# Performance work log

Hardware: AMD Instinct MI355X
Metric: run time of the kernel (lower is better)

The kernel has to match this reference:

```python
import jax, jax.numpy as jnp
import numpy as np

NC = 6            # CPAB tessellation cells (tess_size=6, zero_boundary=True)
DIM = NC - 1      # theta dimension = 5
SIG_LEN = 2048
CHANNELS = 3
BATCH = 256
FC_IN = 64 * 168  # flattened net_part1 output for signal_len=2048
NUM_SCALING = 0   # N in transform_data_ss
EPS_BN = 1e-5


def _cpab_basis():
    """QR null-space basis of the CPAB continuity + zero-boundary constraints.
    Params ordered [a_1,b_1,...,a_NC,b_NC]; v(x)=a_c x + b_c on cell c."""
    nc = NC
    L = np.zeros((nc + 1, 2 * nc))
    for k in range(1, nc):  # continuity at internal knots x_k = k/nc
        xk = k / nc
        L[k - 1, 2 * (k - 1)] = xk
        L[k - 1, 2 * (k - 1) + 1] = 1.0
        L[k - 1, 2 * k] = -xk
        L[k - 1, 2 * k + 1] = -1.0
    L[nc - 1, 1] = 1.0        # v(0) = 0  -> b_1 = 0
    L[nc, 2 * (nc - 1)] = 1.0  # v(1) = 0 -> a_nc + b_nc = 0
    L[nc, 2 * nc - 1] = 1.0
    Q, _ = np.linalg.qr(L.T, mode='complete')
    return np.ascontiguousarray(Q[:, nc + 1:]).astype(np.float32)  # (12, 5)


def _conv1d(x, w, b):
    y = jax.lax.conv_general_dilated(x, w, (1,), 'VALID',
                                     dimension_numbers=('NCH', 'OIH', 'NCH'))
    return y + b[None, :, None]


def _maxpool1d(x, k, s):
    return jax.lax.reduce_window(x, -jnp.inf, jax.lax.max, (1, 1, k), (1, 1, s), 'VALID')


def _bn(x, g, b, m, v):  # eval-mode BatchNorm1d
    return (x - m[None, :, None]) * (g / jnp.sqrt(v + EPS_BN))[None, :, None] + b[None, :, None]


def _integrate(x, A):
    """Exact CPAB 1D flow integration over t=1 with cell-crossing handling.
    x: (B, n) points in [0,1]; A: (B, NC, 2) per-cell (a, b). Monotone
    trajectories cross at most NC-1 boundaries -> fixed NC+1 iterations."""
    a_all, b_all = A[:, :, 0], A[:, :, 1]
    t = jnp.ones_like(x)
    for _ in range(NC + 1):
        c = jnp.clip(jnp.floor(x * NC).astype(jnp.int32), 0, NC - 1)
        a = jnp.take_along_axis(a_all, c, axis=1)
        b = jnp.take_along_axis(b_all, c, axis=1)
        v = a * x + b
        xb = jnp.where(v >= 0, (c + 1).astype(x.dtype) / NC, c.astype(x.dtype) / NC)
        big_a = jnp.abs(a) > 1e-8
        a_s = jnp.where(big_a, a, 1.0)
        z = x + b / a_s        # shifted coord: x(t) = z*exp(a t) - b/a
        zb = xb + b / a_s
        ratio = zb / jnp.where(jnp.abs(z) > 1e-12, z, 1e-12)
        t_exp = jnp.log(jnp.maximum(ratio, 1e-12)) / a_s
        v_s = jnp.where(jnp.abs(v) > 1e-12, v, 1.0)
        t_lin = (xb - x) / v_s
        thit = jnp.where(big_a, t_exp, t_lin)
        valid = (jnp.abs(v) > 1e-12) & (thit > 0) & (jnp.where(big_a, ratio, 1.0) > 0)
        thit = jnp.where(valid, thit, jnp.inf)
        tau = jnp.minimum(t, thit)
        x_new = jnp.where(big_a, z * jnp.exp(a * tau) - (z - x), x + b * tau)
        hit = thit <= t
        nudge = jnp.where(v >= 0, 1e-6, -1e-6)  # push into next cell
        x = jnp.clip(jnp.where(hit, xb + nudge, x_new), 0.0, 1.0)
        t = jnp.maximum(t - tau, 0.0)
    return x


def _interp1d(data, pos):
    """data: (B, L, C); pos: (B, n) in [0,1] -> (B, n, C) linear interpolation."""
    Lw = data.shape[1]
    p = jnp.clip(pos, 0.0, 1.0) * (Lw - 1)
    x0 = jnp.clip(jnp.floor(p).astype(jnp.int32), 0, Lw - 2)
    w = (p - x0.astype(p.dtype))[:, :, None]
    d0 = jnp.take_along_axis(data, x0[:, :, None], axis=1)
    d1 = jnp.take_along_axis(data, (x0 + 1)[:, :, None], axis=1)
    return d0 * (1.0 - w) + d1 * w


def _transform_data_ss(data, theta, basis, outsize, N):
    """CPAB scaling-and-squaring warp of data (B, L, C) by theta (B, DIM)."""
    Bsz = theta.shape[0]
    A = (theta @ basis.T).reshape(Bsz, NC, 2) / (2.0 ** N)
    grid = jnp.linspace(0.0, 1.0, outsize, dtype=data.dtype)
    grid_t = _integrate(jnp.broadcast_to(grid, (Bsz, outsize)), A)
    for _ in range(N):  # squaring: compose the warp with itself
        grid_t = _interp1d(grid_t[:, :, None], grid_t)[:, :, 0]
    return _interp1d(data, grid_t)


def reference(x, conv1_w, conv1_b, bn1_g, bn1_b, bn1_m, bn1_v,
              conv2_w, conv2_b, bn2_g, bn2_b, bn2_m, bn2_v,
              conv3_w, conv3_b, bn3_g, bn3_b, bn3_m, bn3_v,
              fc1_w, fc1_b, fc2_w, fc2_b, fc3_w, fc3_b, fc4_w, fc4_b, basis):
    # localization net (n_recurrence = 1, back_version = True)
    h = jax.nn.relu(_maxpool1d(_bn(_conv1d(x, conv1_w, conv1_b), bn1_g, bn1_b, bn1_m, bn1_v), 3, 2))
    h = jax.nn.relu(_maxpool1d(_bn(_conv1d(h, conv2_w, conv2_b), bn2_g, bn2_b, bn2_m, bn2_v), 3, 3))
    h = jax.nn.relu(_maxpool1d(_bn(_conv1d(h, conv3_w, conv3_b), bn3_g, bn3_b, bn3_m, bn3_v), 3, 2))
    xs = h.reshape(h.shape[0], -1)  # (B, 64*168)
    xs = jax.nn.relu(xs @ fc1_w.T + fc1_b)
    xs = jax.nn.relu(xs @ fc2_w.T + fc2_b)
    xs = jax.nn.relu(xs @ fc3_w.T + fc3_b)
    theta = jnp.tanh(xs @ fc4_w.T + fc4_b)  # (B, 5)
    data = jnp.transpose(x, (0, 2, 1))       # (B, L, C)
    warped = _transform_data_ss(data, theta, basis, SIG_LEN, NUM_SCALING)
    return jnp.transpose(warped, (0, 2, 1))  # (B, C, L)


def setup_inputs() -> dict:
    key = jax.random.key(0)
    ks = jax.random.split(key, 16)
    def nrm(k, shape, scale):
        return (jax.random.normal(k, shape) * scale).astype(jnp.float32)
    inp = {}
    inp['x'] = jax.random.normal(ks[0], (BATCH, CHANNELS, SIG_LEN), dtype=jnp.float32)
    inp['conv1_w'] = nrm(ks[1], (128, CHANNELS, 3), (CHANNELS * 3) ** -0.5)
    inp['conv1_b'] = nrm(ks[2], (128,), 0.01)
    inp['bn1_g'] = jnp.ones((128,), jnp.float32)
    inp['bn1_b'] = jnp.zeros((128,), jnp.float32)
    inp['bn1_m'] = nrm(ks[3], (128,), 0.1)
    inp['bn1_v'] = jnp.ones((128,), jnp.float32)
    inp['conv2_w'] = nrm(ks[4], (64, 128, 5), (128 * 5) ** -0.5)
    inp['conv2_b'] = nrm(ks[5], (64,), 0.01)
    inp['bn2_g'] = jnp.ones((64,), jnp.float32)
    inp['bn2_b'] = jnp.zeros((64,), jnp.float32)
    inp['bn2_m'] = nrm(ks[6], (64,), 0.1)
    inp['bn2_v'] = jnp.ones((64,), jnp.float32)
    inp['conv3_w'] = nrm(ks[7], (64, 64, 3), (64 * 3) ** -0.5)
    inp['conv3_b'] = nrm(ks[8], (64,), 0.01)
    inp['bn3_g'] = jnp.ones((64,), jnp.float32)
    inp['bn3_b'] = jnp.zeros((64,), jnp.float32)
    inp['bn3_m'] = nrm(ks[9], (64,), 0.1)
    inp['bn3_v'] = jnp.ones((64,), jnp.float32)
    inp['fc1_w'] = nrm(ks[10], (48, FC_IN), FC_IN ** -0.5)
    inp['fc1_b'] = jnp.zeros((48,), jnp.float32)
    inp['fc2_w'] = nrm(ks[11], (32, 48), 48 ** -0.5)
    inp['fc2_b'] = jnp.zeros((32,), jnp.float32)
    inp['fc3_w'] = nrm(ks[12], (16, 32), 32 ** -0.5)
    inp['fc3_b'] = jnp.zeros((16,), jnp.float32)
    # near-identity warp head (original zero-inits weight, identity bias)
    inp['fc4_w'] = nrm(ks[13], (DIM, 16), 0.01)
    inp['fc4_b'] = nrm(ks[14], (DIM,), 0.01)
    inp['basis'] = jnp.asarray(_cpab_basis())
    return inp
```

## Files before the change

### kernel.cpp

```cpp
#include <hip/hip_runtime.h>
#include <math.h>

#define BATCH   256
#define SIGLEN  2048
#define L1OUT   1022
#define L2OUT   339
#define L3OUT   168
#define FCIN    10752

#define TP2   32
#define NROW  100
#define PLANE (NROW*128)

#define TU3   28

typedef float f32x4   __attribute__((ext_vector_type(4)));
typedef float f32x16  __attribute__((ext_vector_type(16)));
typedef short s16x8   __attribute__((ext_vector_type(8)));

__device__ __forceinline__ unsigned short f2bf(float f) {
    unsigned int u = __float_as_uint(f);
    return (unsigned short)((u + 0x7fffu + ((u >> 16) & 1u)) >> 16);
}
__device__ __forceinline__ float bf2f(unsigned short h) {
    return __uint_as_float(((unsigned int)h) << 16);
}

__launch_bounds__(256)
__global__ void prep_kernel(
    const float* __restrict__ conv1_b,
    const float* __restrict__ g1, const float* __restrict__ b1,
    const float* __restrict__ m1, const float* __restrict__ v1,
    const float* __restrict__ conv2_w, const float* __restrict__ conv2_b,
    const float* __restrict__ g2, const float* __restrict__ b2,
    const float* __restrict__ m2, const float* __restrict__ v2,
    const float* __restrict__ conv3_w, const float* __restrict__ conv3_b,
    const float* __restrict__ g3, const float* __restrict__ b3,
    const float* __restrict__ m3, const float* __restrict__ v3,
    const float* __restrict__ fc1_w,
    unsigned short* __restrict__ w2hi, unsigned short* __restrict__ w2lo,
    unsigned short* __restrict__ w3hi, unsigned short* __restrict__ w3lo,
    float* __restrict__ wp1,
    float* __restrict__ so1, float* __restrict__ so2, float* __restrict__ so3)
{
    __shared__ float tl[64 * 169];

    int t   = threadIdx.x;
    int tid = blockIdx.x * 256 + t;
    int stride = gridDim.x * 256;

    if (blockIdx.x < 48) {
        int o = blockIdx.x;
        for (int i = t; i < FCIN; i += 256) {
            int co = i / L3OUT, u = i - co * L3OUT;
            tl[co * 169 + u] = fc1_w[o * FCIN + i];
        }
        __syncthreads();
        for (int i = t; i < FCIN; i += 256) {
            int u = i >> 6, co = i & 63;
            wp1[o * FCIN + i] = tl[co * 169 + u];
        }
    }

    for (int i = tid; i < 64*128*5; i += stride) {
        int co = i / 640; int rr = i - co*640; int ci = rr / 5; int k = rr - ci*5;
        float w = conv2_w[i];
        unsigned short hi = f2bf(w);
        unsigned short lo = f2bf(w - bf2f(hi));
        int dst = ((k*8 + (ci >> 4))*64 + co)*16 + (ci & 15);
        w2hi[dst] = hi;
        w2lo[dst] = lo;
    }
    for (int i = tid; i < 64*64*3; i += stride) {
        int co = i / 192; int r = i - co*192; int ci = r / 3; int k = r - ci*3;
        float w = conv3_w[i];
        unsigned short hi = f2bf(w);
        unsigned short lo = f2bf(w - bf2f(hi));
        int dst = ((k*2 + (ci >> 5))*64 + co)*32 + (ci & 31);
        w3hi[dst] = hi;
        w3lo[dst] = lo;
    }
    if (tid < 128) {
        float s = g1[tid] / sqrtf(v1[tid] + 1e-5f);
        so1[tid]       = s;
        so1[128 + tid] = (conv1_b[tid] - m1[tid]) * s + b1[tid];
    }
    if (tid < 64) {
        float s2 = g2[tid] / sqrtf(v2[tid] + 1e-5f);
        so2[tid]      = s2;
        so2[64 + tid] = (conv2_b[tid] - m2[tid]) * s2 + b2[tid];
        float s3 = g3[tid] / sqrtf(v3[tid] + 1e-5f);
        so3[tid]      = s3;
        so3[64 + tid] = (conv3_b[tid] - m3[tid]) * s3 + b3[tid];
    }
}

__launch_bounds__(512, 6)
__global__ void conv12_kernel(
    const float* __restrict__ x, const float* __restrict__ w1,
    const unsigned short* __restrict__ w2hi, const unsigned short* __restrict__ w2lo,
    const float* __restrict__ so1, const float* __restrict__ so2,
    unsigned int* __restrict__ h2p)
{
    __shared__ unsigned short h1[2*PLANE];
    unsigned short* h1hi = h1;
    unsigned short* h1lo = h1 + PLANE;

    int t  = threadIdx.x;
    int b  = blockIdx.x;
    int by = blockIdx.y;
    int u0 = by * TP2;
    int wv = __builtin_amdgcn_readfirstlane(t >> 6);
    int l  = t & 63;

    {
        float wr[2][9], s1r[2], o1r[2];
        #pragma unroll
        for (int h = 0; h < 2; ++h) {
            int ch = 2*l + h;
            #pragma unroll
            for (int j = 0; j < 9; ++j) wr[h][j] = w1[ch*9 + j];
            s1r[h] = so1[ch]; o1r[h] = so1[128 + ch];
        }

        int rbase = 13 * wv;
        int W0 = 192*by + 2*rbase;
        const float* xp0 = x + b*3*SIGLEN;

        float xv[3][6];
        if (W0 + 5 <= SIGLEN - 1) {
            #pragma unroll
            for (int ci = 0; ci < 3; ++ci) {
                const float* xp = xp0 + ci*SIGLEN + W0;
                float2 v01 = *(const float2*)(xp);
                float2 v23 = *(const float2*)(xp + 2);
                float2 v45 = *(const float2*)(xp + 4);
                xv[ci][0] = v01.x; xv[ci][1] = v01.y;
                xv[ci][2] = v23.x; xv[ci][3] = v23.y;
                xv[ci][4] = v45.x; xv[ci][5] = v45.y;
            }
        } else {
            #pragma unroll
            for (int ci = 0; ci < 3; ++ci)
                #pragma unroll
                for (int j = 0; j < 6; ++j) {
                    int xi = W0 + j; xi = xi < SIGLEN ? xi : SIGLEN - 1;
                    xv[ci][j] = xp0[ci*SIGLEN + xi];
                }
        }

        float cr0 = 0.f, cr1 = 0.f;
        #pragma unroll
        for (int s = 0; s < 13; ++s) {
            int r = rbase + s;
            if (r < NROW) {
                float vo[2];
                #pragma unroll
                for (int h = 0; h < 2; ++h) {
                    float r0, r1 = 0.f, r2 = 0.f;
                    if (s == 0) {
                        r0 = 0.f;
                        #pragma unroll
                        for (int ci = 0; ci < 3; ++ci)
                            r0 = fmaf(xv[ci][0], wr[h][ci*3],
                                 fmaf(xv[ci][1], wr[h][ci*3+1],
                                 fmaf(xv[ci][2], wr[h][ci*3+2], r0)));
                    } else {
                        r0 = h ? cr1 : cr0;
                    }
                    #pragma unroll
                    for (int ci = 0; ci < 3; ++ci) {
                        float wA = wr[h][ci*3], wB = wr[h][ci*3+1], wC = wr[h][ci*3+2];
                        r1 = fmaf(xv[ci][1], wA, fmaf(xv[ci][2], wB, fmaf(xv[ci][3], wC, r1)));
                        r2 = fmaf(xv[ci][2], wA, fmaf(xv[ci][3], wB, fmaf(xv[ci][4], wC, r2)));
                    }
                    if (h) cr1 = r2; else cr0 = r2;
                    float mx = fmaxf(r0, fmaxf(r1, r2));
                    vo[h] = fmaxf(fmaf(s1r[h], mx, o1r[h]), 0.f);
                }
                unsigned ua = __float_as_uint(vo[0]);
                unsigned ub = __float_as_uint(vo[1]);
                unsigned hb = ub & 0xffff0000u;
                unsigned hipack = (ua >> 16) | hb;
                float ra = vo[0] - __uint_as_float(ua & 0xffff0000u);
                float rb = vo[1] - __uint_as_float(hb);
                unsigned lopack = (__float_as_uint(ra) >> 16) | (__float_as_uint(rb) & 0xffff0000u);
                int wi = r*64 + (l ^ ((r & 7) << 2));
                ((unsigned*)h1hi)[wi] = hipack;
                ((unsigned*)h1lo)[wi] = lopack;
            }
            if (s < 12) {
                #pragma unroll
                for (int ci = 0; ci < 3; ++ci) {
                    xv[ci][0] = xv[ci][2]; xv[ci][1] = xv[ci][3];
                    xv[ci][2] = xv[ci][4]; xv[ci][3] = xv[ci][5];
                }
                int Wn = W0 + 2*s + 6;
                if (Wn + 1 <= SIGLEN - 1) {
                    #pragma unroll
                    for (int ci = 0; ci < 3; ++ci) {
                        float2 v = *(const float2*)(xp0 + ci*SIGLEN + Wn);
                        xv[ci][4] = v.x; xv[ci][5] = v.y;
                    }
                } else {
                    #pragma unroll
                    for (int ci = 0; ci < 3; ++ci) {
                        int x4 = Wn     < SIGLEN ? Wn     : SIGLEN - 1;
                        int x5 = Wn + 1 < SIGLEN ? Wn + 1 : SIGLEN - 1;
                        xv[ci][4] = xp0[ci*SIGLEN + x4];
                        xv[ci][5] = xp0[ci*SIGLEN + x5];
                    }
                }
            }
        }
    }
    __syncthreads();

    int tid8 = (wv + ((b + by) & 7)) & 7;
    int active = tid8 < 6;
    int mt = tid8 >> 1;
    int nt = tid8 & 1;
    int lm  = l & 31;
    int hi8 = (l >> 5) * 8;

    f32x16 acc = (f32x16)(0.f);
    if (active) {
        const unsigned short* wbh = w2hi + (nt*32 + lm)*16 + hi8;
        const unsigned short* wbl = w2lo + (nt*32 + lm)*16 + hi8;
        #pragma unroll
        for (int k = 0; k < 5; ++k) {
            int row = mt*32 + lm + k;
            int sb  = row*128 + hi8;
            int swz = (row & 7) << 3;
            #pragma unroll
            for (int c16 = 0; c16 < 8; ++c16) {
                int st = k*8 + c16;
                s16x8 wh = *(const s16x8*)(wbh + st*1024);
                s16x8 wl = *(const s16x8*)(wbl + st*1024);
                int idx = (sb + c16*16) ^ swz;
                s16x8 ah = *(const s16x8*)&h1hi[idx];
                s16x8 al = *(const s16x8*)&h1lo[idx];
                acc = __builtin_amdgcn_mfma_f32_32x32x16_bf16(ah, wh, acc, 0, 0, 0);
                acc = __builtin_amdgcn_mfma_f32_32x32x16_bf16(al, wh, acc, 0, 0, 0);
                acc = __builtin_amdgcn_mfma_f32_32x32x16_bf16(ah, wl, acc, 0, 0, 0);
            }
        }
    }
    __syncthreads();

    float* c2 = (float*)h1;
    if (active) {
        #pragma unroll
        for (int rg = 0; rg < 16; ++rg) {
            int prow = mt*32 + (rg & 3) + 8*(rg >> 2) + 4*(l >> 5);
            c2[prow*65 + nt*32 + lm] = acc[rg];
        }
    }
    __syncthreads();

    #pragma unroll
    for (int it = 0; it < 4; ++it) {
        int idx = t + it*512;
        int ul = idx >> 6, co = idx & 63;
        int u = u0 + ul;
        if (u < L2OUT) {
            float v0 = c2[(3*ul  )*65 + co];
            float v1 = c2[(3*ul+1)*65 + co];
            float v2 = c2[(3*ul+2)*65 + co];
            float mm = fmaxf(v0, fmaxf(v1, v2));
            float v  = fmaxf(fmaf(so2[co], mm, so2[64 + co]), 0.f);
            unsigned uu = __float_as_uint(v);
            float rr = v - __uint_as_float(uu & 0xffff0000u);
            h2p[(b*L2OUT + u)*64 + co] = (uu >> 16) | (__float_as_uint(rr) & 0xffff0000u);
        }
    }
}

__launch_bounds__(256, 4)
__global__ void conv3fc1_kernel(
    const unsigned int* __restrict__ h2p,
    const unsigned short* __restrict__ w3hi, const unsigned short* __restrict__ w3lo,
    const float* __restrict__ so3, const float* __restrict__ wp1,
    float* __restrict__ part)
{
    __shared__ unsigned short h3s[2*66*72];
    __shared__ float c3buf[64*65];

    int t  = threadIdx.x;
    int b  = blockIdx.x;
    int ti = blockIdx.y;
    int u0 = ti * TU3;
    int wv = __builtin_amdgcn_readfirstlane(t >> 6);
    int l  = t & 63;
    int m  = l & 15;
    int qd = l >> 4;

    for (int i = t; i < 66*64; i += 256) {
        int r = i >> 6, ci = i & 63;
        int g = 2*u0 + r; g = g > (L2OUT-1) ? (L2OUT-1) : g;
        unsigned int v = h2p[(b*L2OUT + g)*64 + ci];
        h3s[r*72 + ci]         = (unsigned short)(v & 0xffffu);
        h3s[66*72 + r*72 + ci] = (unsigned short)(v >> 16);
    }
    __syncthreads();

    s16x8 wh[6], wl[6];
    #pragma unroll
    for (int s = 0; s < 6; ++s) {
        wh[s] = *(const s16x8*)(w3hi + s*2048 + (wv*16 + m)*32 + qd*8);
        wl[s] = *(const s16x8*)(w3lo + s*2048 + (wv*16 + m)*32 + qd*8);
    }

    f32x4 acc[4] = {(f32x4)(0.f), (f32x4)(0.f), (f32x4)(0.f), (f32x4)(0.f)};
    #pragma unroll
    for (int pt = 0; pt < 4; ++pt) {
        #pragma unroll
        for (int s = 0; s < 6; ++s) {
            int row = pt*16 + m + (s >> 1);
            int off = (s & 1)*32 + qd*8;
            s16x8 ah = *(const s16x8*)&h3s[row*72 + off];
            s16x8 al = *(const s16x8*)&h3s[66*72 + row*72 + off];
            acc[pt] = __builtin_amdgcn_mfma_f32_16x16x32_bf16(ah, wh[s], acc[pt], 0, 0, 0);
            acc[pt] = __builtin_amdgcn_mfma_f32_16x16x32_bf16(al, wh[s], acc[pt], 0, 0, 0);
            acc[pt] = __builtin_amdgcn_mfma_f32_16x16x32_bf16(ah, wl[s], acc[pt], 0, 0, 0);
        }
    }
    __syncthreads();

    #pragma unroll
    for (int pt = 0; pt < 4; ++pt)
        #pragma unroll
        for (int rg = 0; rg < 4; ++rg)
            c3buf[(pt*16 + qd*4 + rg)*65 + wv*16 + m] = acc[pt][rg];
    __syncthreads();

    float s3 = so3[l], o3 = so3[64 + l];
    float pooled[TU3];
    #pragma unroll
    for (int u = 0; u < TU3; ++u) {
        int p = 2*u;
        float v0 = c3buf[(p  )*65 + l];
        float v1 = c3buf[(p+1)*65 + l];
        float v2 = c3buf[(p+2)*65 + l];
        pooled[u] = fmaxf(fmaf(s3, fmaxf(v0, fmaxf(v1, v2)), o3), 0.f);
    }

    int o0 = wv * 12;
    float fa[12];
    #pragma unroll
    for (int j = 0; j < 12; ++j) fa[j] = 0.f;
    #pragma unroll 4
    for (int u = 0; u < TU3; ++u) {
        float pv = pooled[u];
        const float* wp = wp1 + (u0 + u)*64 + l;
        #pragma unroll
        for (int j = 0; j < 12; ++j)
            fa[j] = fmaf(pv, wp[(o0 + j)*FCIN], fa[j]);
    }
    #pragma unroll
    for (int j = 0; j < 12; ++j) {
        #pragma unroll
        for (int off = 32; off > 0; off >>= 1)
            fa[j] += __shfl_xor(fa[j], off, 64);
    }
    if (l == 0) {
        #pragma unroll
        for (int j = 0; j < 12; ++j)
            part[(b*6 + ti)*48 + o0 + j] = fa[j];
    }
}

__launch_bounds__(256)
__global__ void warp_kernel(
    const float* __restrict__ x, const float* __restrict__ part,
    const float* __restrict__ fc1_b,
    const float* __restrict__ fc2_w, const float* __restrict__ fc2_b,
    const float* __restrict__ fc3_w, const float* __restrict__ fc3_b,
    const float* __restrict__ fc4_w, const float* __restrict__ fc4_b,
    const float* __restrict__ basis,
    float* __restrict__ out)
{
    __shared__ float xs48[48], hl[32], gl[16], thl[5], Al[12];

    int b = blockIdx.x;
    int t = threadIdx.x;

    if (t < 48) {
        float sv = 0.f;
        #pragma unroll
        for (int ti = 0; ti < 6; ++ti) sv += part[(b*6 + ti)*48 + t];
        xs48[t] = fmaxf(sv + fc1_b[t], 0.f);
    }
    __syncthreads();
    if (t < 32) {
        float sv = fc2_b[t];
        #pragma unroll
        for (int k = 0; k < 48; ++k) sv = fmaf(fc2_w[t * 48 + k], xs48[k], sv);
        hl[t] = fmaxf(sv, 0.f);
    }
    __syncthreads();
    if (t < 16) {
        float sv = fc3_b[t];
        #pragma unroll
        for (int k = 0; k < 32; ++k) sv = fmaf(fc3_w[t * 32 + k], hl[k], sv);
        gl[t] = fmaxf(sv, 0.f);
    }
    __syncthreads();
    if (t < 5) {
        float sv = fc4_b[t];
        #pragma unroll
        for (int k = 0; k < 16; ++k) sv = fmaf(fc4_w[t * 16 + k], gl[k], sv);
        thl[t] = tanhf(sv);
    }
    __syncthreads();
    if (t < 12) {
        float sv = 0.f;
        #pragma unroll
        for (int d = 0; d < 5; ++d) sv = fmaf(basis[t * 5 + d], thl[d], sv);
        Al[t] = sv;
    }
    __syncthreads();

    float a_r[6], b_r[6];
    #pragma unroll
    for (int c = 0; c < 6; ++c) { a_r[c] = Al[2*c]; b_r[c] = Al[2*c+1]; }

    #pragma unroll
    for (int cc = 0; cc < 2; ++cc) {
        int i = (blockIdx.y * 2 + cc) * 256 + t;
        float xp = (float)i / 2047.f;
        float tt = 1.f;
        for (int it = 0; it < 7; ++it) {
            int c = (int)floorf(xp * 6.f);
            c = min(max(c, 0), 5);
            float a  = a_r[c], bb = b_r[c];
            float v  = a * xp + bb;
            float xb = (v >= 0.f) ? (float)(c + 1) / 6.f : (float)c / 6.f;
            bool  big_a = fabsf(a) > 1e-8f;
            float a_s = big_a ? a : 1.f;
            float z   = xp + bb / a_s;
            float zb  = xb + bb / a_s;
            float zden = (fabsf(z) > 1e-12f) ? z : 1e-12f;
            float ratio = zb / zden;
            float t_exp = logf(fmaxf(ratio, 1e-12f)) / a_s;
            float v_s   = (fabsf(v) > 1e-12f) ? v : 1.f;
            float t_lin = (xb - xp) / v_s;
            float thit  = big_a ? t_exp : t_lin;
            bool valid  = (fabsf(v) > 1e-12f) && (thit > 0.f) && ((big_a ? ratio : 1.f) > 0.f);
            if (!valid) thit = __builtin_inff();
            float tau   = fminf(tt, thit);
            float x_new = big_a ? (z * expf(a * tau) - (z - xp)) : (xp + bb * tau);
            bool hit    = (thit <= tt);
            float nudge = (v >= 0.f) ? 1e-6f : -1e-6f;
            xp = hit ? (xb + nudge) : x_new;
            xp = fminf(fmaxf(xp, 0.f), 1.f);
            tt = fmaxf(tt - tau, 0.f);
        }
        float p = fminf(fmaxf(xp, 0.f), 1.f) * 2047.f;
        int i0 = (int)floorf(p);
        i0 = min(max(i0, 0), 2046);
        float w = p - (float)i0;
        #pragma unroll
        for (int c = 0; c < 3; ++c) {
            const float* d = &x[(b * 3 + c) * SIGLEN];
            out[(b * 3 + c) * SIGLEN + i] = d[i0] * (1.f - w) + d[i0 + 1] * w;
        }
    }
}

extern "C" void kernel_launch(void* const* d_in, const int* in_sizes, int n_in,
                              void* d_out, int out_size, void* d_ws, size_t ws_size,
                              hipStream_t stream) {
    (void)in_sizes; (void)n_in; (void)out_size; (void)ws_size;
    const float* x       = (const float*)d_in[0];
    const float* conv1_w = (const float*)d_in[1];
    const float* conv1_b = (const float*)d_in[2];
    const float* bn1_g   = (const float*)d_in[3];
    const float* bn1_b   = (const float*)d_in[4];
    const float* bn1_m   = (const float*)d_in[5];
    const float* bn1_v   = (const float*)d_in[6];
    const float* conv2_w = (const float*)d_in[7];
    const float* conv2_b = (const float*)d_in[8];
    const float* bn2_g   = (const float*)d_in[9];
    const float* bn2_b   = (const float*)d_in[10];
    const float* bn2_m   = (const float*)d_in[11];
    const float* bn2_v   = (const float*)d_in[12];
    const float* conv3_w = (const float*)d_in[13];
    const float* conv3_b = (const float*)d_in[14];
    const float* bn3_g   = (const float*)d_in[15];
    const float* bn3_b   = (const float*)d_in[16];
    const float* bn3_m   = (const float*)d_in[17];
    const float* bn3_v   = (const float*)d_in[18];
    const float* fc1_w   = (const float*)d_in[19];
    const float* fc1_b   = (const float*)d_in[20];
    const float* fc2_w   = (const float*)d_in[21];
    const float* fc2_b   = (const float*)d_in[22];
    const float* fc3_w   = (const float*)d_in[23];
    const float* fc3_b   = (const float*)d_in[24];
    const float* fc4_w   = (const float*)d_in[25];
    const float* fc4_b   = (const float*)d_in[26];
    const float* basis   = (const float*)d_in[27];

    unsigned short* w2hi = (unsigned short*)d_ws;
    unsigned short* w2lo = w2hi + 40960;
    unsigned short* w3hi = w2lo + 40960;
    unsigned short* w3lo = w3hi + 12288;
    float* ws   = (float*)d_ws;
    float* so1  = ws + 53248;
    float* so2  = so1 + 256;
    float* so3  = so2 + 128;
    float* wp1  = so3 + 128;
    unsigned int* h2p = (unsigned int*)(wp1 + 516096);
    float* part = (float*)(h2p + 5554176);

    prep_kernel<<<128, 256, 0, stream>>>(
        conv1_b, bn1_g, bn1_b, bn1_m, bn1_v,
        conv2_w, conv2_b, bn2_g, bn2_b, bn2_m, bn2_v,
        conv3_w, conv3_b, bn3_g, bn3_b, bn3_m, bn3_v,
        fc1_w, w2hi, w2lo, w3hi, w3lo, wp1, so1, so2, so3);

    dim3 g2(BATCH, (L2OUT + TP2 - 1) / TP2);
    conv12_kernel<<<g2, 512, 0, stream>>>(x, conv1_w, w2hi, w2lo, so1, so2, h2p);

    dim3 g3(BATCH, 6);
    conv3fc1_kernel<<<g3, 256, 0, stream>>>(h2p, w3hi, w3lo, so3, wp1, part);

    dim3 g5(BATCH, 4);
    warp_kernel<<<g5, 256, 0, stream>>>(x, part, fc1_b, fc2_w, fc2_b,
                                        fc3_w, fc3_b, fc4_w, fc4_b, basis,
                                        (float*)d_out);
}
```

Baseline: 250.0 us.

## Split conv2 MFMA work along K across waves and reduce partials in LDS

Each active wave now covers all three M tiles for one third of the 40 K steps, where before it handled one M tile over all K steps. Each B fragment (weight) load is reused across three MFMA tiles and is prefetched one step ahead. The partial accumulators are then combined through an LDS reduction with an extra barrier. This trades fewer global weight loads for triple the accumulator registers, extra LDS traffic and a sync, and the loop is no longer unrolled.

```diff
diff --git a/kernel.cpp b/kernel.cpp
--- a/kernel.cpp
+++ b/kernel.cpp
@@ -218,31 +218,61 @@
 
     int tid8 = (wv + ((b + by) & 7)) & 7;
     int active = tid8 < 6;
-    int mt = tid8 >> 1;
     int nt = tid8 & 1;
+    int j  = tid8 >> 1;
     int lm  = l & 31;
     int hi8 = (l >> 5) * 8;
 
-    f32x16 acc = (f32x16)(0.f);
+    f32x16 acc[3] = {(f32x16)(0.f), (f32x16)(0.f), (f32x16)(0.f)};
     if (active) {
+        int st  = (j == 0) ? 0 : (j == 1 ? 14 : 27);
+        int cnt = (j == 0) ? 14 : 13;
         const unsigned short* wbh = w2hi + (nt*32 + lm)*16 + hi8;
         const unsigned short* wbl = w2lo + (nt*32 + lm)*16 + hi8;
-        #pragma unroll
-        for (int k = 0; k < 5; ++k) {
-            int row = mt*32 + lm + k;
-            int sb  = row*128 + hi8;
-            int swz = (row & 7) << 3;
+        s16x8 wh = *(const s16x8*)(wbh + st*1024);
+        s16x8 wl = *(const s16x8*)(wbl + st*1024);
+        for (int i = 0; i < cnt; ++i) {
+            int stn = st + 1; stn = stn > 39 ? 39 : stn;
+            s16x8 whn = *(const s16x8*)(wbh + stn*1024);
+            s16x8 wln = *(const s16x8*)(wbl + stn*1024);
+            int k = st >> 3, c16 = st & 7;
+            int rb = lm + k;
             #pragma unroll
-            for (int c16 = 0; c16 < 8; ++c16) {
-                int st = k*8 + c16;
-                s16x8 wh = *(const s16x8*)(wbh + st*1024);
-                s16x8 wl = *(const s16x8*)(wbl + st*1024);
-                int idx = (sb + c16*16) ^ swz;
+            for (int mt = 0; mt < 3; ++mt) {
+                int row = mt*32 + rb;
+                int idx = (row*128 + c16*16 + hi8) ^ ((row & 7) << 3);
                 s16x8 ah = *(const s16x8*)&h1hi[idx];
                 s16x8 al = *(const s16x8*)&h1lo[idx];
-                acc = __builtin_amdgcn_mfma_f32_32x32x16_bf16(ah, wh, acc, 0, 0, 0);
-                acc = __builtin_amdgcn_mfma_f32_32x32x16_bf16(al, wh, acc, 0, 0, 0);
-                acc = __builtin_amdgcn_mfma_f32_32x32x16_bf16(ah, wl, acc, 0, 0, 0);
+                acc[mt] = __builtin_amdgcn_mfma_f32_32x32x16_bf16(ah, wh, acc[mt], 0, 0, 0);
+                acc[mt] = __builtin_amdgcn_mfma_f32_32x32x16_bf16(al, wh, acc[mt], 0, 0, 0);
+                acc[mt] = __builtin_amdgcn_mfma_f32_32x32x16_bf16(ah, wl, acc[mt], 0, 0, 0);
+            }
+            wh = whn; wl = wln; st = stn;
+        }
+    }
+    __syncthreads();
+
+    float* P = (float*)h1;
+    if (active) {
+        #pragma unroll
+        for (int mt = 0; mt < 3; ++mt) {
+            if (mt != j) {
+                int slot = ((mt + 1) % 3 == j) ? 0 : 1;
+                float* dst = P + ((nt*3 + mt)*2 + slot)*1024 + l;
+                #pragma unroll
+                for (int rg = 0; rg < 16; ++rg) dst[rg*64] = acc[mt][rg];
+            }
+        }
+    }
+    __syncthreads();
+    if (active) {
+        #pragma unroll
+        for (int mt = 0; mt < 3; ++mt) {
+            if (mt == j) {
+                const float* s0 = P + ((nt*3 + mt)*2 + 0)*1024 + l;
+                #pragma unroll
+                for (int rg = 0; rg < 16; ++rg)
+                    acc[mt][rg] += s0[rg*64] + s0[1024 + rg*64];
             }
         }
     }
@@ -251,9 +281,14 @@
     float* c2 = (float*)h1;
     if (active) {
         #pragma unroll
-        for (int rg = 0; rg < 16; ++rg) {
-            int prow = mt*32 + (rg & 3) + 8*(rg >> 2) + 4*(l >> 5);
-            c2[prow*65 + nt*32 + lm] = acc[rg];
+        for (int mt = 0; mt < 3; ++mt) {
+            if (mt == j) {
+                #pragma unroll
+                for (int rg = 0; rg < 16; ++rg) {
+                    int prow = mt*32 + (rg & 3) + 8*(rg >> 2) + 4*(l >> 5);
+                    c2[prow*65 + nt*32 + lm] = acc[mt][rg];
+                }
+            }
         }
     }
     __syncthreads();
```

Result: no change. 252.6 us (+1.1%).

## Warp-specialize conv12 into persistent per-batch block with double-buffered conv1 producer

Applied to the files above, without the earlier changes.

The conv1+conv2 kernel becomes one 1024-thread block per batch element that walks all 11 position tiles, in place of a 2D grid of 512-thread blocks. Four waves act as producers and compute the next tile's conv1 rows into a double-buffered LDS plane while twelve MFMA waves compute conv2 on the current tile. The conv2 K dimension is split across wave pairs and the halves are summed in LDS. This aims to overlap the scalar conv1 work with matrix-core work and to use all waves, where six of eight were active before. In exchange it adds more barriers, raises LDS use, and gives the grid only 256 blocks.

```diff
diff --git a/kernel.cpp b/kernel.cpp
--- a/kernel.cpp
+++ b/kernel.cpp
@@ -11,6 +11,7 @@
 #define TP2   32
 #define NROW  100
 #define PLANE (NROW*128)
+#define NTILE 11
 
 #define TU3   28
 
@@ -95,26 +96,140 @@
     }
 }
 
-__launch_bounds__(512, 6)
+__device__ __forceinline__ void c1_init_window(const float* xp0, int W0, float xv[3][6])
+{
+    if (W0 + 5 <= SIGLEN - 1) {
+        #pragma unroll
+        for (int ci = 0; ci < 3; ++ci) {
+            const float* xp = xp0 + ci*SIGLEN + W0;
+            float2 v01 = *(const float2*)(xp);
+            float2 v23 = *(const float2*)(xp + 2);
+            float2 v45 = *(const float2*)(xp + 4);
+            xv[ci][0] = v01.x; xv[ci][1] = v01.y;
+            xv[ci][2] = v23.x; xv[ci][3] = v23.y;
+            xv[ci][4] = v45.x; xv[ci][5] = v45.y;
+        }
+    } else {
+        #pragma unroll
+        for (int ci = 0; ci < 3; ++ci)
+            #pragma unroll
+            for (int j = 0; j < 6; ++j) {
+                int xi = W0 + j; xi = xi < SIGLEN ? xi : SIGLEN - 1;
+                xv[ci][j] = xp0[ci*SIGLEN + xi];
+            }
+    }
+}
+
+__device__ __forceinline__ void c1_row(
+    const float* xp0, int W0, int r, bool fresh, bool refill, int s,
+    const float wr[2][9], const float s1r[2], const float o1r[2],
+    float xv[3][6], float& cr0, float& cr1,
+    unsigned* dhi, unsigned* dlo, int l)
+{
+    float vo[2];
+    #pragma unroll
+    for (int h = 0; h < 2; ++h) {
+        float r0;
+        if (fresh) {
+            r0 = 0.f;
+            #pragma unroll
+            for (int ci = 0; ci < 3; ++ci)
+                r0 = fmaf(xv[ci][0], wr[h][ci*3],
+                     fmaf(xv[ci][1], wr[h][ci*3+1],
+                     fmaf(xv[ci][2], wr[h][ci*3+2], r0)));
+        } else {
+            r0 = h ? cr1 : cr0;
+        }
+        float r1 = 0.f, r2 = 0.f;
+        #pragma unroll
+        for (int ci = 0; ci < 3; ++ci) {
+            float wA = wr[h][ci*3], wB = wr[h][ci*3+1], wC = wr[h][ci*3+2];
+            r1 = fmaf(xv[ci][1], wA, fmaf(xv[ci][2], wB, fmaf(xv[ci][3], wC, r1)));
+            r2 = fmaf(xv[ci][2], wA, fmaf(xv[ci][3], wB, fmaf(xv[ci][4], wC, r2)));
+        }
+        if (h) cr1 = r2; else cr0 = r2;
+        float mx = fmaxf(r0, fmaxf(r1, r2));
+        vo[h] = fmaxf(fmaf(s1r[h], mx, o1r[h]), 0.f);
+    }
+    unsigned ua = __float_as_uint(vo[0]);
+    unsigned ub = __float_as_uint(vo[1]);
+    unsigned hb = ub & 0xffff0000u;
+    unsigned hipack = (ua >> 16) | hb;
+    float ra = vo[0] - __uint_as_float(ua & 0xffff0000u);
+    float rb = vo[1] - __uint_as_float(hb);
+    unsigned lopack = (__float_as_uint(ra) >> 16) | (__float_as_uint(rb) & 0xffff0000u);
+    int wi = r*64 + (l ^ ((r & 7) << 2));
+    dhi[wi] = hipack;
+    dlo[wi] = lopack;
+    if (refill) {
+        #pragma unroll
+        for (int ci = 0; ci < 3; ++ci) {
+            xv[ci][0] = xv[ci][2]; xv[ci][1] = xv[ci][3];
+            xv[ci][2] = xv[ci][4]; xv[ci][3] = xv[ci][5];
+        }
+        int Wn = W0 + 2*s + 6;
+        if (Wn + 1 <= SIGLEN - 1) {
+            #pragma unroll
+            for (int ci = 0; ci < 3; ++ci) {
+                float2 v = *(const float2*)(xp0 + ci*SIGLEN + Wn);
+                xv[ci][4] = v.x; xv[ci][5] = v.y;
+            }
+        } else {
+            #pragma unroll
+            for (int ci = 0; ci < 3; ++ci) {
+                int x4 = Wn     < SIGLEN ? Wn     : SIGLEN - 1;
+                int x5 = Wn + 1 < SIGLEN ? Wn + 1 : SIGLEN - 1;
+                xv[ci][4] = xp0[ci*SIGLEN + x4];
+                xv[ci][5] = xp0[ci*SIGLEN + x5];
+            }
+        }
+    }
+}
+
+__device__ __forceinline__ void c1_seg(
+    int s0, int s1, int tile, int g, int l, const float* xp0,
+    const float wr[2][9], const float s1r[2], const float o1r[2],
+    float xv[3][6], float& cr0, float& cr1,
+    unsigned short* bhi, unsigned short* blo)
+{
+    int rbase = g * 25;
+    int W0 = 192*tile + 2*rbase;
+    unsigned* dhi = (unsigned*)bhi;
+    unsigned* dlo = (unsigned*)blo;
+    if (s0 == 0) {
+        c1_init_window(xp0, W0, xv);
+        c1_row(xp0, W0, rbase, true, true, 0, wr, s1r, o1r, xv, cr0, cr1, dhi, dlo, l);
+        for (int s = 1; s < s1; ++s)
+            c1_row(xp0, W0, rbase + s, false, true, s, wr, s1r, o1r, xv, cr0, cr1, dhi, dlo, l);
+    } else {
+        for (int s = s0; s < s1; ++s)
+            c1_row(xp0, W0, rbase + s, false, s < 24, s, wr, s1r, o1r, xv, cr0, cr1, dhi, dlo, l);
+    }
+}
+
+__launch_bounds__(1024, 4)
 __global__ void conv12_kernel(
     const float* __restrict__ x, const float* __restrict__ w1,
     const unsigned short* __restrict__ w2hi, const unsigned short* __restrict__ w2lo,
     const float* __restrict__ so1, const float* __restrict__ so2,
     unsigned int* __restrict__ h2p)
 {
-    __shared__ unsigned short h1[2*PLANE];
-    unsigned short* h1hi = h1;
-    unsigned short* h1lo = h1 + PLANE;
+    __shared__ unsigned short h1[2][2*PLANE];
+    __shared__ float c2s[96*65];
 
     int t  = threadIdx.x;
     int b  = blockIdx.x;
-    int by = blockIdx.y;
-    int u0 = by * TP2;
     int wv = __builtin_amdgcn_readfirstlane(t >> 6);
     int l  = t & 63;
 
-    {
-        float wr[2][9], s1r[2], o1r[2];
+    float so2s = so2[t & 63], so2o = so2[64 + (t & 63)];
+
+    float wr[2][9], s1r[2], o1r[2];
+    float xv[3][6];
+    float cr0 = 0.f, cr1 = 0.f;
+    int g = wv - 12;
+    const float* xp0 = x + b*3*SIGLEN;
+    if (wv >= 12) {
         #pragma unroll
         for (int h = 0; h < 2; ++h) {
             int ch = 2*l + h;
@@ -122,157 +237,86 @@
             for (int j = 0; j < 9; ++j) wr[h][j] = w1[ch*9 + j];
             s1r[h] = so1[ch]; o1r[h] = so1[128 + ch];
         }
-
-        int rbase = 13 * wv;
-        int W0 = 192*by + 2*rbase;
-        const float* xp0 = x + b*3*SIGLEN;
-
-        float xv[3][6];
-        if (W0 + 5 <= SIGLEN - 1) {
-            #pragma unroll
-            for (int ci = 0; ci < 3; ++ci) {
-                const float* xp = xp0 + ci*SIGLEN + W0;
-                float2 v01 = *(const float2*)(xp);
-                float2 v23 = *(const float2*)(xp + 2);
-                float2 v45 = *(const float2*)(xp + 4);
-                xv[ci][0] = v01.x; xv[ci][1] = v01.y;
-                xv[ci][2] = v23.x; xv[ci][3] = v23.y;
-                xv[ci][4] = v45.x; xv[ci][5] = v45.y;
-            }
-        } else {
-            #pragma unroll
-            for (int ci = 0; ci < 3; ++ci)
-                #pragma unroll
-                for (int j = 0; j < 6; ++j) {
-                    int xi = W0 + j; xi = xi < SIGLEN ? xi : SIGLEN - 1;
-                    xv[ci][j] = xp0[ci*SIGLEN + xi];
-                }
-        }
-
-        float cr0 = 0.f, cr1 = 0.f;
-        #pragma unroll
-        for (int s = 0; s < 13; ++s) {
-            int r = rbase + s;
-            if (r < NROW) {
-                float vo[2];
-                #pragma unroll
-                for (int h = 0; h < 2; ++h) {
-                    float r0, r1 = 0.f, r2 = 0.f;
-                    if (s == 0) {
-                        r0 = 0.f;
-                        #pragma unroll
-                        for (int ci = 0; ci < 3; ++ci)
-                            r0 = fmaf(xv[ci][0], wr[h][ci*3],
-                                 fmaf(xv[ci][1], wr[h][ci*3+1],
-                                 fmaf(xv[ci][2], wr[h][ci*3+2], r0)));
-                    } else {
-                        r0 = h ? cr1 : cr0;
-                    }
-                    #pragma unroll
-                    for (int ci = 0; ci < 3; ++ci) {
-                        float wA = wr[h][ci*3], wB = wr[h][ci*3+1], wC = wr[h][ci*3+2];
-                        r1 = fmaf(xv[ci][1], wA, fmaf(xv[ci][2], wB, fmaf(xv[ci][3], wC, r1)));
-                        r2 = fmaf(xv[ci][2], wA, fmaf(xv[ci][3], wB, fmaf(xv[ci][4], wC, r2)));
-                    }
-                    if (h) cr1 = r2; else cr0 = r2;
-                    float mx = fmaxf(r0, fmaxf(r1, r2));
-                    vo[h] = fmaxf(fmaf(s1r[h], mx, o1r[h]), 0.f);
-                }
-                unsigned ua = __float_as_uint(vo[0]);
-                unsigned ub = __float_as_uint(vo[1]);
-                unsigned hb = ub & 0xffff0000u;
-                unsigned hipack = (ua >> 16) | hb;
-                float ra = vo[0] - __uint_as_float(ua & 0xffff0000u);
-                float rb = vo[1] - __uint_as_float(hb);
-                unsigned lopack = (__float_as_uint(ra) >> 16) | (__float_as_uint(rb) & 0xffff0000u);
-                int wi = r*64 + (l ^ ((r & 7) << 2));
-                ((unsigned*)h1hi)[wi] = hipack;
-                ((unsigned*)h1lo)[wi] = lopack;
-            }
-            if (s < 12) {
-                #pragma unroll
-                for (int ci = 0; ci < 3; ++ci) {
-                    xv[ci][0] = xv[ci][2]; xv[ci][1] = xv[ci][3];
-                    xv[ci][2] = xv[ci][4]; xv[ci][3] = xv[ci][5];
-                }
-                int Wn = W0 + 2*s + 6;
-                if (Wn + 1 <= SIGLEN - 1) {
-                    #pragma unroll
-                    for (int ci = 0; ci < 3; ++ci) {
-                        float2 v = *(const float2*)(xp0 + ci*SIGLEN + Wn);
-                        xv[ci][4] = v.x; xv[ci][5] = v.y;
-                    }
-                } else {
-                    #pragma unroll
-                    for (int ci = 0; ci < 3; ++ci) {
-                        int x4 = Wn     < SIGLEN ? Wn     : SIGLEN - 1;
-                        int x5 = Wn + 1 < SIGLEN ? Wn + 1 : SIGLEN - 1;
-                        xv[ci][4] = xp0[ci*SIGLEN + x4];
-                        xv[ci][5] = xp0[ci*SIGLEN + x5];
-                    }
-                }
-            }
-        }
-    }
-    __syncthreads();
-
-    int tid8 = (wv + ((b + by) & 7)) & 7;
-    int active = tid8 < 6;
-    int mt = tid8 >> 1;
-    int nt = tid8 & 1;
+    }
+    int mt = wv >> 2;
+    int nt = (wv >> 1) & 1;
+    int ks = wv & 1;
     int lm  = l & 31;
     int hi8 = (l >> 5) * 8;
-
-    f32x16 acc = (f32x16)(0.f);
-    if (active) {
-        const unsigned short* wbh = w2hi + (nt*32 + lm)*16 + hi8;
-        const unsigned short* wbl = w2lo + (nt*32 + lm)*16 + hi8;
-        #pragma unroll
-        for (int k = 0; k < 5; ++k) {
-            int row = mt*32 + lm + k;
-            int sb  = row*128 + hi8;
-            int swz = (row & 7) << 3;
+    const unsigned short* wbh = w2hi + ks*20480 + (nt*32 + lm)*16 + hi8;
+    const unsigned short* wbl = w2lo + ks*20480 + (nt*32 + lm)*16 + hi8;
+
+    if (wv >= 12)
+        c1_seg(0, 25, 0, g, l, xp0, wr, s1r, o1r, xv, cr0, cr1, h1[0], h1[0] + PLANE);
+    __syncthreads();
+
+    for (int tl = 0; tl < NTILE; ++tl) {
+        f32x16 acc;
+        if (wv < 12) {
+            acc = (f32x16)(0.f);
+            const unsigned short* chi = h1[tl & 1];
+            const unsigned short* clo = chi + PLANE;
+            int kofs = ks * 20;
             #pragma unroll
-            for (int c16 = 0; c16 < 8; ++c16) {
-                int st = k*8 + c16;
-                s16x8 wh = *(const s16x8*)(wbh + st*1024);
-                s16x8 wl = *(const s16x8*)(wbl + st*1024);
-                int idx = (sb + c16*16) ^ swz;
-                s16x8 ah = *(const s16x8*)&h1hi[idx];
-                s16x8 al = *(const s16x8*)&h1lo[idx];
+            for (int i = 0; i < 20; ++i) {
+                int st  = kofs + i;
+                int k   = st >> 3;
+                int c16 = st & 7;
+                int row = mt*32 + lm + k;
+                int idx = (row*128 + c16*16 + hi8) ^ ((row & 7) << 3);
+                s16x8 wh = *(const s16x8*)(wbh + i*1024);
+                s16x8 wl = *(const s16x8*)(wbl + i*1024);
+                s16x8 ah = *(const s16x8*)&chi[idx];
+                s16x8 al = *(const s16x8*)&clo[idx];
                 acc = __builtin_amdgcn_mfma_f32_32x32x16_bf16(ah, wh, acc, 0, 0, 0);
                 acc = __builtin_amdgcn_mfma_f32_32x32x16_bf16(al, wh, acc, 0, 0, 0);
                 acc = __builtin_amdgcn_mfma_f32_32x32x16_bf16(ah, wl, acc, 0, 0, 0);
             }
-        }
-    }
-    __syncthreads();
-
-    float* c2 = (float*)h1;
-    if (active) {
-        #pragma unroll
-        for (int rg = 0; rg < 16; ++rg) {
-            int prow = mt*32 + (rg & 3) + 8*(rg >> 2) + 4*(l >> 5);
-            c2[prow*65 + nt*32 + lm] = acc[rg];
-        }
-    }
-    __syncthreads();
-
-    #pragma unroll
-    for (int it = 0; it < 4; ++it) {
-        int idx = t + it*512;
-        int ul = idx >> 6, co = idx & 63;
-        int u = u0 + ul;
-        if (u < L2OUT) {
-            float v0 = c2[(3*ul  )*65 + co];
-            float v1 = c2[(3*ul+1)*65 + co];
-            float v2 = c2[(3*ul+2)*65 + co];
-            float mm = fmaxf(v0, fmaxf(v1, v2));
-            float v  = fmaxf(fmaf(so2[co], mm, so2[64 + co]), 0.f);
-            unsigned uu = __float_as_uint(v);
-            float rr = v - __uint_as_float(uu & 0xffff0000u);
-            h2p[(b*L2OUT + u)*64 + co] = (uu >> 16) | (__float_as_uint(rr) & 0xffff0000u);
-        }
+            if (ks == 0) {
+                #pragma unroll
+                for (int rg = 0; rg < 16; ++rg) {
+                    int prow = mt*32 + (rg & 3) + 8*(rg >> 2) + 4*(l >> 5);
+                    c2s[prow*65 + nt*32 + lm] = acc[rg];
+                }
+            }
+        } else if (tl < NTILE - 1) {
+            c1_seg(0, 13, tl + 1, g, l, xp0, wr, s1r, o1r, xv, cr0, cr1,
+                   h1[(tl + 1) & 1], h1[(tl + 1) & 1] + PLANE);
+        }
+        __syncthreads();
+
+        if (wv < 12) {
+            if (ks == 1) {
+                #pragma unroll
+                for (int rg = 0; rg < 16; ++rg) {
+                    int prow = mt*32 + (rg & 3) + 8*(rg >> 2) + 4*(l >> 5);
+                    int ci = prow*65 + nt*32 + lm;
+                    c2s[ci] += acc[rg];
+                }
+            }
+        } else if (tl < NTILE - 1) {
+            c1_seg(13, 25, tl + 1, g, l, xp0, wr, s1r, o1r, xv, cr0, cr1,
+                   h1[(tl + 1) & 1], h1[(tl + 1) & 1] + PLANE);
+        }
+        __syncthreads();
+
+        #pragma unroll
+        for (int it = 0; it < 2; ++it) {
+            int idx = t + it*1024;
+            int ul = idx >> 6, co = idx & 63;
+            int u = tl*TP2 + ul;
+            if (u < L2OUT) {
+                float v0 = c2s[(3*ul  )*65 + co];
+                float v1 = c2s[(3*ul+1)*65 + co];
+                float v2 = c2s[(3*ul+2)*65 + co];
+                float mm = fmaxf(v0, fmaxf(v1, v2));
+                float v  = fmaxf(fmaf(so2s, mm, so2o), 0.f);
+                unsigned uu = __float_as_uint(v);
+                float rr = v - __uint_as_float(uu & 0xffff0000u);
+                h2p[(b*L2OUT + u)*64 + co] = (uu >> 16) | (__float_as_uint(rr) & 0xffff0000u);
+            }
+        }
+        __syncthreads();
     }
 }
 
@@ -519,8 +563,7 @@
         conv3_w, conv3_b, bn3_g, bn3_b, bn3_m, bn3_v,
         fc1_w, w2hi, w2lo, w3hi, w3lo, wp1, so1, so2, so3);
 
-    dim3 g2(BATCH, (L2OUT + TP2 - 1) / TP2);
-    conv12_kernel<<<g2, 512, 0, stream>>>(x, conv1_w, w2hi, w2lo, so1, so2, h2p);
+    conv12_kernel<<<BATCH, 1024, 0, stream>>>(x, conv1_w, w2hi, w2lo, so1, so2, h2p);
 
     dim3 g3(BATCH, 6);
     conv3fc1_kernel<<<g3, 256, 0, stream>>>(h2p, w3hi, w3lo, so3, wp1, part);
```

New measurement: 380.2 us. 1.52x slower.
